# Kernel optimization log

Measured on AMD Instinct MI355X. Metric: run time of the kernel, lower is better.

Reference implementation:

```python
import jax, jax.numpy as jnp
import numpy as np

SAMPLE_SIZE = 512
DOE_DIM = 10
LATENT = 32
BATCH = 8192
HID = SAMPLE_SIZE // 4   # 128
HID2 = SAMPLE_SIZE // 2  # 256


def _build_groups():
    """Replicates the encoder's per-row neighbor gather construction.
    Returns padded index table [G, Kmax] (int32) and float mask [G, Kmax]."""
    rng = np.random.RandomState(42)
    doe = rng.rand(SAMPLE_SIZE, DOE_DIM)
    sorted_doe = np.argsort(doe, axis=0)  # [S, D]
    idx_list = []
    for i in range(1, SAMPLE_SIZE - 1):
        idxs = np.unique(sorted_doe[i - 1:i + 2, :].flatten())
        idx_list.append(idxs)
    G = len(idx_list)               # sample_size - 2 = 510
    K = max(len(a) for a in idx_list)  # <= 3 * DOE_DIM
    idx = np.zeros((G, K), dtype=np.int32)
    mask = np.zeros((G, K), dtype=np.float32)
    for g, a in enumerate(idx_list):
        idx[g, :len(a)] = a
        mask[g, :len(a)] = 1.0
    return jnp.asarray(idx), jnp.asarray(mask)


def _dense_init(key, fan_in, fan_out):
    w = jax.random.normal(key, (fan_in, fan_out), dtype=jnp.float32) / jnp.sqrt(jnp.float32(fan_in))
    b = jnp.zeros((fan_out,), dtype=jnp.float32)
    return w, b


def setup_inputs() -> dict:
    key = jax.random.key(0)
    ks = jax.random.split(key, 8)
    idx, mask = _build_groups()
    G, K = idx.shape
    x = jax.random.uniform(ks[0], (BATCH, SAMPLE_SIZE), dtype=jnp.float32)
    # per-group Dense(1): weight [G, K] (padded slots zeroed by mask), bias [G]
    gw = jax.random.normal(ks[1], (G, K), dtype=jnp.float32) / jnp.sqrt(jnp.float32(K))
    gb = jnp.zeros((G,), dtype=jnp.float32)
    w1, b1 = _dense_init(ks[2], G, HID)
    w2, b2 = _dense_init(ks[3], HID, LATENT)
    dw1, db1 = _dense_init(ks[4], LATENT, HID)
    dw2, db2 = _dense_init(ks[5], HID, HID2)
    dw3, db3 = _dense_init(ks[6], HID2, SAMPLE_SIZE)
    return {"x": x, "gw": gw, "gb": gb, "w1": w1, "b1": b1, "w2": w2, "b2": b2,
            "dw1": dw1, "db1": db1, "dw2": dw2, "db2": db2, "dw3": dw3, "db3": db3,
            "idx": idx, "mask": mask}


def reference(x, gw, gb, w1, b1, w2, b2, dw1, db1, dw2, db2, dw3, db3, idx, mask):
    # Encoder: grouped gather + per-group Dense(1, relu), fused as one einsum.
    gathered = x[:, idx]                                   # [B, G, K]
    h = jax.nn.relu(jnp.einsum('bgk,gk->bg', gathered, gw * mask) + gb)  # [B, G]
    h = jax.nn.relu(h @ w1 + b1)                           # [B, ss/4]
    z = jax.nn.relu(h @ w2 + b2)                           # [B, latent]
    # Decoder MLP
    d = jax.nn.relu(z @ dw1 + db1)                         # [B, ss/4]
    d = jax.nn.relu(d @ dw2 + db2)                         # [B, ss/2]
    out = jax.nn.sigmoid(d @ dw3 + db3)                    # [B, ss]
    return out
```

## Files before the change

### kernel.cpp

```cpp
#include <hip/hip_runtime.h>
#include <hip/hip_bf16.h>

#define SAMPLE 512
#define GDIM   510
#define HID    128
#define LATENT 32
#define HID2   256
#define TB     32
#define NT     512

typedef unsigned short u16;
typedef unsigned int   u32;
typedef __attribute__((ext_vector_type(8))) short s16x8;
typedef __attribute__((ext_vector_type(4))) float f32x4;

#define WGP_OFF   0
#define W1P_OFF   (WGP_OFF  + 32*16*512)
#define W2P_OFF   (W1P_OFF  + 8*16*512)
#define DW1P_OFF  (W2P_OFF  + 2*4*512)
#define DW2P_OFF  (DW1P_OFF + 8*1*512)
#define DW3P_OFF  (DW2P_OFF + 16*4*512)
#define PACK_U16  (DW3P_OFF + 32*8*512)
#define NCHUNK    (PACK_U16 / 8)

__device__ __forceinline__ u16 f2b(float f) {
    union { float f; u32 i; } v; v.f = f;
    return (u16)((v.i + 0x7FFFu + ((v.i >> 16) & 1u)) >> 16);
}

__global__ __launch_bounds__(256) void build_ws(
    const float* __restrict__ w1, const float* __restrict__ w2,
    const float* __restrict__ dw1, const float* __restrict__ dw2,
    const float* __restrict__ dw3,
    const float* __restrict__ gw, const float* __restrict__ mask,
    const int* __restrict__ idx,
    u16* __restrict__ ws, int G, int K)
{
    int c = blockIdx.x * 256 + threadIdx.x;
    if (c >= NCHUNK) return;
    u16 tmp[8];
    if (c < W1P_OFF / 8) {
        int lane = c & 63;
        int kt   = (c >> 6) & 15;
        int nt   = (c >> 6) >> 4;
        int g    = nt * 16 + (lane & 15);
        int k0   = kt * 32 + (lane >> 4) * 8;
        #pragma unroll
        for (int j = 0; j < 8; ++j) tmp[j] = 0;
        if (g < G) {
            const int*   idxr = idx  + (size_t)g * K;
            const float* gwr  = gw   + (size_t)g * K;
            const float* mr   = mask + (size_t)g * K;
            for (int t = 0; t < K; ++t) {
                int j = idxr[t] - k0;
                float m = mr[t];
                if ((unsigned)j < 8u && m > 0.f) tmp[j] = f2b(gwr[t] * m);
            }
        }
        *(s16x8*)(ws + (size_t)c * 8) = *(s16x8*)tmp;
        return;
    }
    const float* W; int Kd, Nd, KT, base;
    if      (c < W2P_OFF / 8)  { W = w1;  Kd = GDIM;   Nd = HID;    KT = 16; base = W1P_OFF / 8; }
    else if (c < DW1P_OFF / 8) { W = w2;  Kd = HID;    Nd = LATENT; KT = 4;  base = W2P_OFF / 8; }
    else if (c < DW2P_OFF / 8) { W = dw1; Kd = LATENT; Nd = HID;    KT = 1;  base = DW1P_OFF / 8; }
    else if (c < DW3P_OFF / 8) { W = dw2; Kd = HID;    Nd = HID2;   KT = 4;  base = DW2P_OFF / 8; }
    else                       { W = dw3; Kd = HID2;   Nd = SAMPLE; KT = 8;  base = DW3P_OFF / 8; }
    int c2   = c - base;
    int lane = c2 & 63;
    int kt   = (c2 >> 6) % KT;
    int nt   = (c2 >> 6) / KT;
    int n    = nt * 16 + (lane & 15);
    int k0   = kt * 32 + (lane >> 4) * 8;
    #pragma unroll
    for (int j = 0; j < 8; ++j) {
        int k = k0 + j;
        float v = (k < Kd && n < Nd) ? W[(size_t)k * Nd + n] : 0.f;
        tmp[j] = f2b(v);
    }
    *(s16x8*)(ws + (size_t)c * 8) = *(s16x8*)tmp;
}

template<int KT, int NTN, int TPW>
__device__ __forceinline__ void mfma_phase(
    int wave, int lane,
    const u16* inl, int sin,
    const u16* __restrict__ pW,
    const float* bias,
    u16* outl, int sout)
{
    if (NTN < 8 && wave >= NTN) return;
    const u16* arow0 = inl + (lane & 15) * sin + (lane >> 4) * 8;
    const u16* arow1 = arow0 + 16 * sin;
    f32x4 acc[TPW][2];
    #pragma unroll
    for (int i = 0; i < TPW; ++i) {
        acc[i][0] = (f32x4){0.f, 0.f, 0.f, 0.f};
        acc[i][1] = (f32x4){0.f, 0.f, 0.f, 0.f};
    }
    #pragma unroll
    for (int kt = 0; kt < KT; ++kt) {
        s16x8 a0 = *(const s16x8*)(arow0 + kt * 32);
        s16x8 a1 = *(const s16x8*)(arow1 + kt * 32);
        #pragma unroll
        for (int i = 0; i < TPW; ++i) {
            int nt = wave + 8 * i;
            s16x8 b = *(const s16x8*)(pW + (size_t)((nt * KT + kt) * 64 + lane) * 8);
            acc[i][0] = __builtin_amdgcn_mfma_f32_16x16x32_bf16(a0, b, acc[i][0], 0, 0, 0);
            acc[i][1] = __builtin_amdgcn_mfma_f32_16x16x32_bf16(a1, b, acc[i][1], 0, 0, 0);
        }
    }
    #pragma unroll
    for (int i = 0; i < TPW; ++i) {
        int nt = wave + 8 * i;
        int col = nt * 16 + (lane & 15);
        float bs = bias[col];
        #pragma unroll
        for (int mt = 0; mt < 2; ++mt) {
            #pragma unroll
            for (int r = 0; r < 4; ++r) {
                int row = mt * 16 + (lane >> 4) * 4 + r;
                float v = acc[i][mt][r] + bs;
                outl[row * sout + col] = f2b(v > 0.f ? v : 0.f);
            }
        }
    }
}

#define XS_OFF 0
#define H2_OFF 0
#define ZZ_OFF 4352
#define D1_OFF 5632
#define D2_OFF 9984
#define H1_OFF 18432
#define SMEM_U16 35072

__global__ __launch_bounds__(NT, 4) void ae_mfma(
    const float* __restrict__ x,
    const float* __restrict__ gb,  const float* __restrict__ b1,
    const float* __restrict__ b2,  const float* __restrict__ db1,
    const float* __restrict__ db2, const float* __restrict__ db3,
    const u16*   __restrict__ ws,
    float* __restrict__ out)
{
    __shared__ __align__(16) u16 smem[SMEM_U16];
    __shared__ float biases[1568];
    u16* xs = smem + XS_OFF;
    u16* h1 = smem + H1_OFF;
    u16* h2 = smem + H2_OFF;
    u16* zz = smem + ZZ_OFF;
    u16* d1 = smem + D1_OFF;
    u16* d2 = smem + D2_OFF;

    const int tid  = threadIdx.x;
    const int wave = tid >> 6;
    const int lane = tid & 63;
    const int b0   = blockIdx.x * TB;

    biases[tid]        = (tid < GDIM) ? gb[tid] : 0.f;
    biases[1056 + tid] = db3[tid];
    if (tid < 128) biases[512 + tid] = b1[tid];
    if (tid < 32)  biases[640 + tid] = b2[tid];
    if (tid < 128) biases[672 + tid] = db1[tid];
    if (tid < 256) biases[800 + tid] = db2[tid];

    {
        const float4* xg = (const float4*)(x + (size_t)b0 * SAMPLE);
        #pragma unroll
        for (int it = 0; it < (TB * SAMPLE / 4) / NT; ++it) {
            int v = it * NT + tid;
            float4 f = xg[v];
            int row = v >> 7;
            int cp  = (v & 127) * 4;
            u16* p = xs + row * 520 + cp;
            u16 t4[4] = { f2b(f.x), f2b(f.y), f2b(f.z), f2b(f.w) };
            *(unsigned long long*)p = *(unsigned long long*)t4;
        }
    }
    __syncthreads();

    mfma_phase<16, 32, 4>(wave, lane, xs, 520, ws + WGP_OFF,  biases,       h1, 520);
    __syncthreads();
    mfma_phase<16, 8, 1>(wave, lane, h1, 520, ws + W1P_OFF,  biases + 512, h2, 136);
    __syncthreads();
    mfma_phase<4, 2, 1>(wave, lane, h2, 136, ws + W2P_OFF,  biases + 640, zz, 40);
    __syncthreads();
    mfma_phase<1, 8, 1>(wave, lane, zz, 40,  ws + DW1P_OFF, biases + 672, d1, 136);
    __syncthreads();
    mfma_phase<4, 16, 2>(wave, lane, d1, 136, ws + DW2P_OFF, biases + 800, d2, 264);
    __syncthreads();

    {
        const u16* arow0 = d2 + (lane & 15) * 264 + (lane >> 4) * 8;
        const u16* arow1 = arow0 + 16 * 264;
        const u16* pW = ws + DW3P_OFF;
        f32x4 acc[4][2];
        #pragma unroll
        for (int i = 0; i < 4; ++i) {
            acc[i][0] = (f32x4){0.f, 0.f, 0.f, 0.f};
            acc[i][1] = (f32x4){0.f, 0.f, 0.f, 0.f};
        }
        #pragma unroll
        for (int kt = 0; kt < 8; ++kt) {
            s16x8 a0 = *(const s16x8*)(arow0 + kt * 32);
            s16x8 a1 = *(const s16x8*)(arow1 + kt * 32);
            #pragma unroll
            for (int i = 0; i < 4; ++i) {
                int nt = wave + 8 * i;
                s16x8 b = *(const s16x8*)(pW + (size_t)((nt * 8 + kt) * 64 + lane) * 8);
                acc[i][0] = __builtin_amdgcn_mfma_f32_16x16x32_bf16(a0, b, acc[i][0], 0, 0, 0);
                acc[i][1] = __builtin_amdgcn_mfma_f32_16x16x32_bf16(a1, b, acc[i][1], 0, 0, 0);
            }
        }
        #pragma unroll
        for (int i = 0; i < 4; ++i) {
            int nt = wave + 8 * i;
            int col = nt * 16 + (lane & 15);
            float bs = biases[1056 + col];
            #pragma unroll
            for (int mt = 0; mt < 2; ++mt) {
                #pragma unroll
                for (int r = 0; r < 4; ++r) {
                    int row = mt * 16 + (lane >> 4) * 4 + r;
                    float v = acc[i][mt][r] + bs;
                    out[(size_t)(b0 + row) * SAMPLE + col] = 1.f / (1.f + __expf(-v));
                }
            }
        }
    }
}

extern "C" void kernel_launch(void* const* d_in, const int* in_sizes, int n_in,
                              void* d_out, int out_size, void* d_ws, size_t ws_size,
                              hipStream_t stream) {
    const float* x   = (const float*)d_in[0];
    const float* gw  = (const float*)d_in[1];
    const float* gb  = (const float*)d_in[2];
    const float* w1  = (const float*)d_in[3];
    const float* b1  = (const float*)d_in[4];
    const float* w2  = (const float*)d_in[5];
    const float* b2  = (const float*)d_in[6];
    const float* dw1 = (const float*)d_in[7];
    const float* db1 = (const float*)d_in[8];
    const float* dw2 = (const float*)d_in[9];
    const float* db2 = (const float*)d_in[10];
    const float* dw3 = (const float*)d_in[11];
    const float* db3 = (const float*)d_in[12];
    const int* idx   = (const int*)d_in[13];
    const float* mask= (const float*)d_in[14];
    float* out = (float*)d_out;
    u16* ws = (u16*)d_ws;

    const int B  = in_sizes[0] / SAMPLE;
    const int G  = in_sizes[2];
    const int K  = in_sizes[1] / G;

    build_ws<<<(NCHUNK + 255) / 256, 256, 0, stream>>>(w1, w2, dw1, dw2, dw3,
                                                       gw, mask, idx, ws, G, K);
    ae_mfma<<<B / TB, NT, 0, stream>>>(x, gb, b1, b2, db1, db2, db3, ws, out);
}
```

Before: 126.2 us.

## Fuse latent and first decoder layers into two-wave path, relax launch bounds

Replaces the two small mfma_phase calls for the latent layer and first decoder layer with a single block in which waves 0 and 1 each handle one 16-row tile through both layers. This removes one block-wide barrier and the per-wave work distribution of those tiny GEMMs. It also relaxes launch bounds from 4 to 2 blocks per CU, which allows more registers at the cost of possible occupancy, and unrolls the weight-packing loop by four. Six of the eight waves sit idle during the fused section.

```diff
diff --git a/kernel.cpp b/kernel.cpp
--- a/kernel.cpp
+++ b/kernel.cpp
@@ -51,7 +51,20 @@
             const int*   idxr = idx  + (size_t)g * K;
             const float* gwr  = gw   + (size_t)g * K;
             const float* mr   = mask + (size_t)g * K;
-            for (int t = 0; t < K; ++t) {
+            int t = 0;
+            for (; t + 4 <= K; t += 4) {
+                int   j0 = idxr[t]     - k0, j1 = idxr[t + 1] - k0;
+                int   j2 = idxr[t + 2] - k0, j3 = idxr[t + 3] - k0;
+                float m0 = mr[t],     m1 = mr[t + 1];
+                float m2 = mr[t + 2], m3 = mr[t + 3];
+                float v0 = gwr[t],     v1 = gwr[t + 1];
+                float v2 = gwr[t + 2], v3 = gwr[t + 3];
+                if ((unsigned)j0 < 8u && m0 > 0.f) tmp[j0] = f2b(v0 * m0);
+                if ((unsigned)j1 < 8u && m1 > 0.f) tmp[j1] = f2b(v1 * m1);
+                if ((unsigned)j2 < 8u && m2 > 0.f) tmp[j2] = f2b(v2 * m2);
+                if ((unsigned)j3 < 8u && m3 > 0.f) tmp[j3] = f2b(v3 * m3);
+            }
+            for (; t < K; ++t) {
                 int j = idxr[t] - k0;
                 float m = mr[t];
                 if ((unsigned)j < 8u && m > 0.f) tmp[j] = f2b(gwr[t] * m);
@@ -135,7 +148,7 @@
 #define H1_OFF 18432
 #define SMEM_U16 35072
 
-__global__ __launch_bounds__(NT, 4) void ae_mfma(
+__global__ __launch_bounds__(NT, 2) void ae_mfma(
     const float* __restrict__ x,
     const float* __restrict__ gb,  const float* __restrict__ b1,
     const float* __restrict__ b2,  const float* __restrict__ db1,
@@ -183,10 +196,62 @@
     __syncthreads();
     mfma_phase<16, 8, 1>(wave, lane, h1, 520, ws + W1P_OFF,  biases + 512, h2, 136);
     __syncthreads();
-    mfma_phase<4, 2, 1>(wave, lane, h2, 136, ws + W2P_OFF,  biases + 640, zz, 40);
-    __syncthreads();
-    mfma_phase<1, 8, 1>(wave, lane, zz, 40,  ws + DW1P_OFF, biases + 672, d1, 136);
-    __syncthreads();
+
+    if (wave < 2) {
+        const int mt = wave;
+        {
+            const u16* arow = h2 + (mt * 16 + (lane & 15)) * 136 + (lane >> 4) * 8;
+            const u16* pW = ws + W2P_OFF;
+            f32x4 acc[2];
+            acc[0] = (f32x4){0.f, 0.f, 0.f, 0.f};
+            acc[1] = (f32x4){0.f, 0.f, 0.f, 0.f};
+            #pragma unroll
+            for (int kt = 0; kt < 4; ++kt) {
+                s16x8 a = *(const s16x8*)(arow + kt * 32);
+                #pragma unroll
+                for (int i = 0; i < 2; ++i) {
+                    s16x8 b = *(const s16x8*)(pW + (size_t)((i * 4 + kt) * 64 + lane) * 8);
+                    acc[i] = __builtin_amdgcn_mfma_f32_16x16x32_bf16(a, b, acc[i], 0, 0, 0);
+                }
+            }
+            #pragma unroll
+            for (int i = 0; i < 2; ++i) {
+                int col = i * 16 + (lane & 15);
+                float bs = biases[640 + col];
+                #pragma unroll
+                for (int r = 0; r < 4; ++r) {
+                    int row = mt * 16 + (lane >> 4) * 4 + r;
+                    float v = acc[i][r] + bs;
+                    zz[row * 40 + col] = f2b(v > 0.f ? v : 0.f);
+                }
+            }
+        }
+        {
+            const u16* arow = zz + (mt * 16 + (lane & 15)) * 40 + (lane >> 4) * 8;
+            const u16* pW = ws + DW1P_OFF;
+            s16x8 a = *(const s16x8*)(arow);
+            f32x4 acc[8];
+            #pragma unroll
+            for (int i = 0; i < 8; ++i) {
+                s16x8 b = *(const s16x8*)(pW + (size_t)(i * 64 + lane) * 8);
+                acc[i] = __builtin_amdgcn_mfma_f32_16x16x32_bf16(
+                    a, b, (f32x4){0.f, 0.f, 0.f, 0.f}, 0, 0, 0);
+            }
+            #pragma unroll
+            for (int i = 0; i < 8; ++i) {
+                int col = i * 16 + (lane & 15);
+                float bs = biases[672 + col];
+                #pragma unroll
+                for (int r = 0; r < 4; ++r) {
+                    int row = mt * 16 + (lane >> 4) * 4 + r;
+                    float v = acc[i][r] + bs;
+                    d1[row * 136 + col] = f2b(v > 0.f ? v : 0.f);
+                }
+            }
+        }
+    }
+    __syncthreads();
+
     mfma_phase<4, 16, 2>(wave, lane, d1, 136, ws + DW2P_OFF, biases + 800, d2, 264);
     __syncthreads();
 
```

New measurement: 119.4 us. 1.06x faster.

## Stage packed weights through LDS in chunks, one MFMA tile per wave

Applied to the files above, without the earlier changes.

Each layer's weight operand now goes into a 64 KB shared-memory buffer, one chunk of 4 N-tiles at a time, with block-wide barriers around every chunk. Each wave then computes a single 16x16 output tile from LDS instead of streaming B fragments from global memory. This lowers launch bounds to 2 blocks per SM, since shared memory use roughly triples. The weight-packing prep loop is also unrolled by 4. The cost is many more barriers, serialized copy-then-compute with no overlap, lower occupancy, and half the waves idle in small layers.

```diff
diff --git a/kernel.cpp b/kernel.cpp
--- a/kernel.cpp
+++ b/kernel.cpp
@@ -51,7 +51,20 @@
             const int*   idxr = idx  + (size_t)g * K;
             const float* gwr  = gw   + (size_t)g * K;
             const float* mr   = mask + (size_t)g * K;
-            for (int t = 0; t < K; ++t) {
+            int t = 0;
+            for (; t + 4 <= K; t += 4) {
+                int   j0 = idxr[t]     - k0, j1 = idxr[t + 1] - k0;
+                int   j2 = idxr[t + 2] - k0, j3 = idxr[t + 3] - k0;
+                float m0 = mr[t],     m1 = mr[t + 1];
+                float m2 = mr[t + 2], m3 = mr[t + 3];
+                float v0 = gwr[t],     v1 = gwr[t + 1];
+                float v2 = gwr[t + 2], v3 = gwr[t + 3];
+                if ((unsigned)j0 < 8u && m0 > 0.f) tmp[j0] = f2b(v0 * m0);
+                if ((unsigned)j1 < 8u && m1 > 0.f) tmp[j1] = f2b(v1 * m1);
+                if ((unsigned)j2 < 8u && m2 > 0.f) tmp[j2] = f2b(v2 * m2);
+                if ((unsigned)j3 < 8u && m3 > 0.f) tmp[j3] = f2b(v3 * m3);
+            }
+            for (; t < K; ++t) {
                 int j = idxr[t] - k0;
                 float m = mr[t];
                 if ((unsigned)j < 8u && m > 0.f) tmp[j] = f2b(gwr[t] * m);
@@ -81,49 +94,52 @@
     *(s16x8*)(ws + (size_t)c * 8) = *(s16x8*)tmp;
 }
 
-template<int KT, int NTN, int TPW>
-__device__ __forceinline__ void mfma_phase(
-    int wave, int lane,
+template<int KT, int NTN, int CN, int SIG>
+__device__ __forceinline__ void mfma_phase_c(
+    int tid, int wave, int lane,
     const u16* inl, int sin,
-    const u16* __restrict__ pW,
+    const u16* __restrict__ pW, u16* wbuf,
     const float* bias,
-    u16* outl, int sout)
+    u16* outl, int sout,
+    float* fout, int b0)
 {
-    if (NTN < 8 && wave >= NTN) return;
-    const u16* arow0 = inl + (lane & 15) * sin + (lane >> 4) * 8;
-    const u16* arow1 = arow0 + 16 * sin;
-    f32x4 acc[TPW][2];
-    #pragma unroll
-    for (int i = 0; i < TPW; ++i) {
-        acc[i][0] = (f32x4){0.f, 0.f, 0.f, 0.f};
-        acc[i][1] = (f32x4){0.f, 0.f, 0.f, 0.f};
-    }
-    #pragma unroll
-    for (int kt = 0; kt < KT; ++kt) {
-        s16x8 a0 = *(const s16x8*)(arow0 + kt * 32);
-        s16x8 a1 = *(const s16x8*)(arow1 + kt * 32);
-        #pragma unroll
-        for (int i = 0; i < TPW; ++i) {
-            int nt = wave + 8 * i;
-            s16x8 b = *(const s16x8*)(pW + (size_t)((nt * KT + kt) * 64 + lane) * 8);
-            acc[i][0] = __builtin_amdgcn_mfma_f32_16x16x32_bf16(a0, b, acc[i][0], 0, 0, 0);
-            acc[i][1] = __builtin_amdgcn_mfma_f32_16x16x32_bf16(a1, b, acc[i][1], 0, 0, 0);
-        }
-    }
-    #pragma unroll
-    for (int i = 0; i < TPW; ++i) {
-        int nt = wave + 8 * i;
-        int col = nt * 16 + (lane & 15);
-        float bs = bias[col];
-        #pragma unroll
-        for (int mt = 0; mt < 2; ++mt) {
+    constexpr int NCH = NTN / CN;
+    constexpr int CHU = CN * KT * 512;
+    const int nt_l = wave % CN;
+    const int mt   = (wave / CN) & 1;
+    const bool act = wave < 2 * CN;
+    const u16* arow = inl + (mt * 16 + (lane & 15)) * sin + (lane >> 4) * 8;
+
+    for (int c = 0; c < NCH; ++c) {
+        {
+            const u16* src = pW + (size_t)c * CHU;
+            for (int off = tid * 8; off < CHU; off += NT * 8)
+                *(s16x8*)(wbuf + off) = *(const s16x8*)(src + off);
+        }
+        __syncthreads();
+        if (act) {
+            f32x4 acc = (f32x4){0.f, 0.f, 0.f, 0.f};
+            #pragma unroll
+            for (int kt = 0; kt < KT; ++kt) {
+                s16x8 a = *(const s16x8*)(arow + kt * 32);
+                s16x8 b = *(const s16x8*)(wbuf + ((nt_l * KT + kt) * 64 + lane) * 8);
+                acc = __builtin_amdgcn_mfma_f32_16x16x32_bf16(a, b, acc, 0, 0, 0);
+            }
+            int nt  = c * CN + nt_l;
+            int col = nt * 16 + (lane & 15);
+            float bs = bias[col];
             #pragma unroll
             for (int r = 0; r < 4; ++r) {
                 int row = mt * 16 + (lane >> 4) * 4 + r;
-                float v = acc[i][mt][r] + bs;
-                outl[row * sout + col] = f2b(v > 0.f ? v : 0.f);
-            }
-        }
+                float v = acc[r] + bs;
+                if (SIG) {
+                    fout[(size_t)(b0 + row) * SAMPLE + col] = 1.f / (1.f + __expf(-v));
+                } else {
+                    outl[row * sout + col] = f2b(v > 0.f ? v : 0.f);
+                }
+            }
+        }
+        __syncthreads();
     }
 }
 
@@ -134,8 +150,9 @@
 #define D2_OFF 9984
 #define H1_OFF 18432
 #define SMEM_U16 35072
-
-__global__ __launch_bounds__(NT, 4) void ae_mfma(
+#define WBUF_U16 32768
+
+__global__ __launch_bounds__(NT, 2) void ae_mfma(
     const float* __restrict__ x,
     const float* __restrict__ gb,  const float* __restrict__ b1,
     const float* __restrict__ b2,  const float* __restrict__ db1,
@@ -144,6 +161,7 @@
     float* __restrict__ out)
 {
     __shared__ __align__(16) u16 smem[SMEM_U16];
+    __shared__ __align__(16) u16 wbuf[WBUF_U16];
     __shared__ float biases[1568];
     u16* xs = smem + XS_OFF;
     u16* h1 = smem + H1_OFF;
@@ -177,57 +195,19 @@
             *(unsigned long long*)p = *(unsigned long long*)t4;
         }
     }
-    __syncthreads();
-
-    mfma_phase<16, 32, 4>(wave, lane, xs, 520, ws + WGP_OFF,  biases,       h1, 520);
-    __syncthreads();
-    mfma_phase<16, 8, 1>(wave, lane, h1, 520, ws + W1P_OFF,  biases + 512, h2, 136);
-    __syncthreads();
-    mfma_phase<4, 2, 1>(wave, lane, h2, 136, ws + W2P_OFF,  biases + 640, zz, 40);
-    __syncthreads();
-    mfma_phase<1, 8, 1>(wave, lane, zz, 40,  ws + DW1P_OFF, biases + 672, d1, 136);
-    __syncthreads();
-    mfma_phase<4, 16, 2>(wave, lane, d1, 136, ws + DW2P_OFF, biases + 800, d2, 264);
-    __syncthreads();
-
-    {
-        const u16* arow0 = d2 + (lane & 15) * 264 + (lane >> 4) * 8;
-        const u16* arow1 = arow0 + 16 * 264;
-        const u16* pW = ws + DW3P_OFF;
-        f32x4 acc[4][2];
-        #pragma unroll
-        for (int i = 0; i < 4; ++i) {
-            acc[i][0] = (f32x4){0.f, 0.f, 0.f, 0.f};
-            acc[i][1] = (f32x4){0.f, 0.f, 0.f, 0.f};
-        }
-        #pragma unroll
-        for (int kt = 0; kt < 8; ++kt) {
-            s16x8 a0 = *(const s16x8*)(arow0 + kt * 32);
-            s16x8 a1 = *(const s16x8*)(arow1 + kt * 32);
-            #pragma unroll
-            for (int i = 0; i < 4; ++i) {
-                int nt = wave + 8 * i;
-                s16x8 b = *(const s16x8*)(pW + (size_t)((nt * 8 + kt) * 64 + lane) * 8);
-                acc[i][0] = __builtin_amdgcn_mfma_f32_16x16x32_bf16(a0, b, acc[i][0], 0, 0, 0);
-                acc[i][1] = __builtin_amdgcn_mfma_f32_16x16x32_bf16(a1, b, acc[i][1], 0, 0, 0);
-            }
-        }
-        #pragma unroll
-        for (int i = 0; i < 4; ++i) {
-            int nt = wave + 8 * i;
-            int col = nt * 16 + (lane & 15);
-            float bs = biases[1056 + col];
-            #pragma unroll
-            for (int mt = 0; mt < 2; ++mt) {
-                #pragma unroll
-                for (int r = 0; r < 4; ++r) {
-                    int row = mt * 16 + (lane >> 4) * 4 + r;
-                    float v = acc[i][mt][r] + bs;
-                    out[(size_t)(b0 + row) * SAMPLE + col] = 1.f / (1.f + __expf(-v));
-                }
-            }
-        }
-    }
+
+    mfma_phase_c<16, 32, 4, 0>(tid, wave, lane, xs, 520, ws + WGP_OFF, wbuf,
+                               biases,       h1, 520, out, b0);
+    mfma_phase_c<16, 8, 4, 0>(tid, wave, lane, h1, 520, ws + W1P_OFF, wbuf,
+                              biases + 512, h2, 136, out, b0);
+    mfma_phase_c<4, 2, 2, 0>(tid, wave, lane, h2, 136, ws + W2P_OFF, wbuf,
+                             biases + 640, zz, 40, out, b0);
+    mfma_phase_c<1, 8, 4, 0>(tid, wave, lane, zz, 40, ws + DW1P_OFF, wbuf,
+                             biases + 672, d1, 136, out, b0);
+    mfma_phase_c<4, 16, 4, 0>(tid, wave, lane, d1, 136, ws + DW2P_OFF, wbuf,
+                              biases + 800, d2, 264, out, b0);
+    mfma_phase_c<8, 32, 4, 1>(tid, wave, lane, d2, 264, ws + DW3P_OFF, wbuf,
+                              biases + 1056, (u16*)nullptr, 0, out, b0);
 }
 
 extern "C" void kernel_launch(void* const* d_in, const int* in_sizes, int n_in,
```

Result: slower. 138.5 us (+9.8%).
